# Optimization experiments

Measured on AMD Instinct MI355X. Metric: run time of the kernel, lower is better.

The kernel has to match this reference:

```python
import jax, jax.numpy as jnp
import numpy as np

# BitLinear (BitNet-style) constants, reconstructed from missing helpers:
#   get_qb_range(b) -> (-2^(b-1), 2^(b-1));  Qb = 2^(b-1) = 128 for bit_range=8
#   get_beta(W)  = mean(|W|)   (||W||_1 / (n*m))
#   get_gamma(W) = max(|W|)
QB = 128.0
EP = 0.01        # ep init arg: clip margin
LN_EPS = 1e-5    # nn.LayerNorm default eps
N_IN = 4096
N_OUT = 4096


def setup_inputs() -> dict:
    key = jax.random.key(0)
    kx, kw = jax.random.split(key, 2)
    x = jax.random.normal(kx, (4, 2048, N_IN), dtype=jnp.float32)
    # weight_init(): w0 ~ N(0,1); alpha = mean(w0); binarize sign(w0 - alpha)
    w0 = jax.random.normal(kw, (N_IN, N_OUT), dtype=jnp.float32)
    alpha = jnp.mean(w0)
    beta = jnp.mean(jnp.abs(w0))          # get_beta
    gamma = jnp.max(jnp.abs(w0))          # get_gamma
    w = jnp.where(w0 - alpha > 0, 1.0, -1.0).astype(jnp.float32)
    ln_gamma = jnp.ones((N_IN,), dtype=jnp.float32)   # LayerNorm weight
    ln_beta = jnp.zeros((N_IN,), dtype=jnp.float32)   # LayerNorm bias
    return {"x": x, "w": w, "ln_gamma": ln_gamma, "ln_beta": ln_beta,
            "beta": beta, "gamma": gamma}


def reference(x, w, ln_gamma, ln_beta, beta, gamma):
    # LayerNorm over last dim
    mu = jnp.mean(x, axis=-1, keepdims=True)
    var = jnp.mean(jnp.square(x - mu), axis=-1, keepdims=True)
    xn = (x - mu) * jax.lax.rsqrt(var + LN_EPS) * ln_gamma + ln_beta
    # ABSMax quantize: scale by Qb/gamma, clip to [-Qb+ep, Qb-ep] (no int cast)
    xq = jnp.clip(xn * (QB / gamma), -QB + EP, QB - EP)
    # binary-weight matmul + dequant scale beta*gamma/Qb
    y = jnp.einsum("bsi,io->bso", xq, w) * (beta * gamma / QB)
    return y
```

## Files before the change

### kernel.cpp

```cpp
#include <hip/hip_runtime.h>

using i32x4  = __attribute__((ext_vector_type(4))) int;
using i32x16 = __attribute__((ext_vector_type(16))) int;

constexpr int K_DIM = 4096;
constexpr int N_DIM = 4096;
constexpr float QBf = 128.0f;
constexpr float EPf = 0.01f;
constexpr float LN_EPSf = 1e-5f;

#define GLOAD_LDS16(gp, lp)                                                  \
    __builtin_amdgcn_global_load_lds(                                        \
        (const __attribute__((address_space(1))) void*)(gp),                 \
        (__attribute__((address_space(3))) void*)(lp), 16, 0, 0)

#define BARRIER()                                                            \
    do { asm volatile("" ::: "memory");                                      \
         __builtin_amdgcn_s_barrier();                                       \
         asm volatile("" ::: "memory"); } while (0)

#define WAIT_LGKM(N)                                                         \
    do { asm volatile("s_waitcnt lgkmcnt(" #N ")" ::: "memory");             \
         __builtin_amdgcn_sched_barrier(0); } while (0)

__global__ __launch_bounds__(256) void ln_quant_kernel(
    const float* __restrict__ x,
    const float* __restrict__ ln_g,
    const float* __restrict__ ln_b,
    const float* __restrict__ gamma_p,
    char* __restrict__ xq)
{
    const int row = blockIdx.x;
    const int t = threadIdx.x;
    const float4* xr4 = reinterpret_cast<const float4*>(x + (size_t)row * K_DIM);

    float4 v[4];
    float sum = 0.f, sumsq = 0.f;
#pragma unroll
    for (int i = 0; i < 4; ++i) {
        v[i] = xr4[t * 4 + i];
        sum += v[i].x + v[i].y + v[i].z + v[i].w;
        sumsq += v[i].x * v[i].x + v[i].y * v[i].y + v[i].z * v[i].z + v[i].w * v[i].w;
    }
#pragma unroll
    for (int off = 32; off > 0; off >>= 1) {
        sum += __shfl_down(sum, off);
        sumsq += __shfl_down(sumsq, off);
    }
    __shared__ float s_sum[4], s_sq[4];
    const int lane = t & 63, w = t >> 6;
    if (lane == 0) { s_sum[w] = sum; s_sq[w] = sumsq; }
    __syncthreads();
    sum = s_sum[0] + s_sum[1] + s_sum[2] + s_sum[3];
    sumsq = s_sq[0] + s_sq[1] + s_sq[2] + s_sq[3];

    const float mu = sum * (1.0f / K_DIM);
    const float var = sumsq * (1.0f / K_DIM) - mu * mu;
    const float rstd = rsqrtf(var + LN_EPSf);
    const float qs = QBf / gamma_p[0];
    const float lo = -QBf + EPf, hi = QBf - EPf;

    alignas(16) char ob[16];
#pragma unroll
    for (int i = 0; i < 4; ++i) {
        const float4 g = reinterpret_cast<const float4*>(ln_g)[t * 4 + i];
        const float4 b = reinterpret_cast<const float4*>(ln_b)[t * 4 + i];
        const float f0 = fminf(fmaxf(((v[i].x - mu) * rstd * g.x + b.x) * qs, lo), hi);
        const float f1 = fminf(fmaxf(((v[i].y - mu) * rstd * g.y + b.y) * qs, lo), hi);
        const float f2 = fminf(fmaxf(((v[i].z - mu) * rstd * g.z + b.z) * qs, lo), hi);
        const float f3 = fminf(fmaxf(((v[i].w - mu) * rstd * g.w + b.w) * qs, lo), hi);
        int x0 = (int)rintf(f0), x1 = (int)rintf(f1);
        int x2 = (int)rintf(f2), x3 = (int)rintf(f3);
        ob[i * 4 + 0] = (char)(x0 > 127 ? 127 : x0);
        ob[i * 4 + 1] = (char)(x1 > 127 ? 127 : x1);
        ob[i * 4 + 2] = (char)(x2 > 127 ? 127 : x2);
        ob[i * 4 + 3] = (char)(x3 > 127 ? 127 : x3);
    }
    *reinterpret_cast<uint4*>(xq + (size_t)row * K_DIM + t * 16) =
        *reinterpret_cast<const uint4*>(ob);
}

__global__ __launch_bounds__(256) void wtrans_kernel(
    const float* __restrict__ w, char* __restrict__ wq)
{
    __shared__ char tile[64][68];
    const int t = threadIdx.x;
    const int bk = blockIdx.y * 64;
    const int bn = blockIdx.x * 64;
#pragma unroll
    for (int i = 0; i < 4; ++i) {
        const int li = i * 1024 + t * 4;
        const int r = li >> 6, c = li & 63;
        const float4 vv = *reinterpret_cast<const float4*>(
            w + (size_t)(bk + r) * N_DIM + bn + c);
        tile[r][c]     = (char)vv.x;
        tile[r][c + 1] = (char)vv.y;
        tile[r][c + 2] = (char)vv.z;
        tile[r][c + 3] = (char)vv.w;
    }
    __syncthreads();
    const int n = t >> 2, kc = t & 3;
    alignas(16) char h16[16];
#pragma unroll
    for (int j = 0; j < 16; ++j) h16[j] = tile[kc * 16 + j][n];
    *reinterpret_cast<uint4*>(wq + (size_t)(bn + n) * K_DIM + bk + kc * 16) =
        *reinterpret_cast<const uint4*>(h16);
}

__global__ __launch_bounds__(512, 2) void gemm_kernel(
    const char* __restrict__ A,
    const char* __restrict__ Bt,
    float* __restrict__ C,
    const float* __restrict__ beta_p,
    const float* __restrict__ gamma_p)
{
    constexpr int NT = K_DIM / 64;
    __shared__ __align__(16) char lds[98304];

    const int t = threadIdx.x;
    const int flat = blockIdx.y * gridDim.x + blockIdx.x;
    const int xcd = flat & 7;
    const int r8 = flat >> 3;
    const int by = ((xcd >> 1) << 3) + (r8 >> 3);
    const int bx = ((xcd & 1) << 3) + (r8 & 7);
    const int bm = by * 256;
    const int bn = bx * 256;

    const int lane = t & 63;
    const int w = t >> 6;
    const int wm = w >> 2;
    const int wn = w & 3;
    const int ln31 = lane & 31;
    const int lg2 = lane >> 5;

    const char* gA = A + (size_t)bm * K_DIM;
    const char* gB = Bt + (size_t)bn * K_DIM;
    const int voff = (t & 255) * K_DIM + ((t >> 8) << 4);

    const int aoff = lg2 * 4096 + ((wm * 128 + ln31) << 4);
    const int boff = lg2 * 4096 + ((wn * 64 + ln31) << 4);

#define STAGE(B, kt)                                                          \
    do {                                                                      \
        GLOAD_LDS16(gA + (size_t)(kt) * 64 + voff,                            \
                    lds + (B) * 32768 + t * 16);                              \
        GLOAD_LDS16(gA + (size_t)(kt) * 64 + voff + 32,                       \
                    lds + (B) * 32768 + 8192 + t * 16);                       \
        GLOAD_LDS16(gB + (size_t)(kt) * 64 + voff,                            \
                    lds + (B) * 32768 + 16384 + t * 16);                      \
        GLOAD_LDS16(gB + (size_t)(kt) * 64 + voff + 32,                       \
                    lds + (B) * 32768 + 16384 + 8192 + t * 16);               \
    } while (0)

#define LD(p) (*reinterpret_cast<const i32x4*>(p))

#define READ_B(BUFI)                                                          \
    do {                                                                      \
        const char* bb_ = lds + (BUFI) * 32768 + 16384;                       \
        _Pragma("unroll")                                                     \
        for (int ks = 0; ks < 2; ++ks)                                        \
            _Pragma("unroll")                                                 \
            for (int nf = 0; nf < 2; ++nf)                                    \
                bfr[ks * 2 + nf] = LD(bb_ + ks * 8192 + nf * 512 + boff);     \
    } while (0)

#define READ_AH(PN, BUFI)                                                     \
    do {                                                                      \
        const char* an_ = lds + (BUFI) * 32768;                               \
        _Pragma("unroll")                                                     \
        for (int ks = 0; ks < 2; ++ks)                                        \
            _Pragma("unroll")                                                 \
            for (int mf = 0; mf < 4; ++mf)                                    \
                afr[PN][ks * 4 + mf] = LD(an_ + ks * 8192 + mf * 512 + aoff); \
    } while (0)

#define MFMA16(P)                                                             \
    do {                                                                      \
        __builtin_amdgcn_s_setprio(1);                                        \
        _Pragma("unroll")                                                     \
        for (int ks = 0; ks < 2; ++ks)                                        \
            _Pragma("unroll")                                                 \
            for (int mf = 0; mf < 4; ++mf)                                    \
                _Pragma("unroll")                                             \
                for (int nf = 0; nf < 2; ++nf)                                \
                    acc[mf][nf] = __builtin_amdgcn_mfma_i32_32x32x32_i8(      \
                        afr[P][ks * 4 + mf], bfr[ks * 2 + nf],                \
                        acc[mf][nf], 0, 0, 0);                                \
        __builtin_amdgcn_s_setprio(0);                                        \
    } while (0)

#define TILE(BC, BN_, BS, P, PN, RD, ST, tt)                                  \
    do {                                                                      \
        READ_B(BC);                                                           \
        if (RD) READ_AH(PN, BN_);                                             \
        if (ST) STAGE(BS, (tt) + 2);                                          \
        if (RD) { WAIT_LGKM(8); } else { WAIT_LGKM(0); }                      \
        MFMA16(P);                                                            \
        asm volatile("s_waitcnt vmcnt(0)" ::: "memory");                      \
        BARRIER();                                                            \
    } while (0)

    i32x16 acc[4][2];
#pragma unroll
    for (int m = 0; m < 4; ++m)
#pragma unroll
        for (int n = 0; n < 2; ++n)
#pragma unroll
            for (int q = 0; q < 16; ++q)
                acc[m][n][q] = 0;

    i32x4 afr[2][8];
    i32x4 bfr[4];

    STAGE(0, 0); STAGE(1, 1);
    asm volatile("s_waitcnt vmcnt(0)" ::: "memory");
    BARRIER();
    READ_AH(0, 0);

    for (int kt = 0; kt < NT - 4; kt += 6) {
        TILE(0, 1, 2, 0, 1, 1, 1, kt);
        TILE(1, 2, 0, 1, 0, 1, 1, kt + 1);
        TILE(2, 0, 1, 0, 1, 1, 1, kt + 2);
        TILE(0, 1, 2, 1, 0, 1, 1, kt + 3);
        TILE(1, 2, 0, 0, 1, 1, 1, kt + 4);
        TILE(2, 0, 1, 1, 0, 1, 1, kt + 5);
    }
    TILE(0, 1, 2, 0, 1, 1, 1, NT - 4);
    TILE(1, 2, 0, 1, 0, 1, 1, NT - 3);
    TILE(2, 0, 1, 0, 1, 1, 0, NT - 2);
    TILE(0, 1, 2, 1, 0, 0, 0, NT - 1);

    const float scale = beta_p[0] * gamma_p[0] * (1.0f / QBf);
    const int orow0 = bm + wm * 128 + lg2 * 4;
    const int ocol0 = bn + wn * 64 + ln31;
#pragma unroll
    for (int mf = 0; mf < 4; ++mf) {
#pragma unroll
        for (int nf = 0; nf < 2; ++nf) {
#pragma unroll
            for (int reg = 0; reg < 16; ++reg) {
                const int row = orow0 + mf * 32 + (reg & 3) + 8 * (reg >> 2);
                C[(size_t)row * N_DIM + ocol0 + nf * 32] =
                    (float)acc[mf][nf][reg] * scale;
            }
        }
    }
#undef STAGE
#undef LD
#undef READ_B
#undef READ_AH
#undef MFMA16
#undef TILE
}

extern "C" void kernel_launch(void* const* d_in, const int* in_sizes, int n_in,
                              void* d_out, int out_size, void* d_ws, size_t ws_size,
                              hipStream_t stream)
{
    const float* x       = (const float*)d_in[0];
    const float* w       = (const float*)d_in[1];
    const float* ln_g    = (const float*)d_in[2];
    const float* ln_b    = (const float*)d_in[3];
    const float* beta_p  = (const float*)d_in[4];
    const float* gamma_p = (const float*)d_in[5];
    float* out = (float*)d_out;

    const int M = in_sizes[0] / K_DIM;

    char* xq = (char*)d_ws;
    char* wq = (char*)d_ws + (size_t)M * K_DIM;

    ln_quant_kernel<<<M, 256, 0, stream>>>(x, ln_g, ln_b, gamma_p, xq);
    wtrans_kernel<<<dim3(N_DIM / 64, K_DIM / 64), 256, 0, stream>>>(w, wq);
    gemm_kernel<<<dim3(N_DIM / 256, M / 256), 512, 0, stream>>>(xq, wq, out, beta_p, gamma_p);
}
```

Measured before the change: 262.2 us.

## Split A/B LDS staging with deeper B prefetch and interleaved A-fragment reads

Restructures the int8 GEMM main loop so A and B tiles get separate LDS ring buffers. A is double-buffered, while B is quad-buffered and prefetched three tiles ahead. A fragments are now read in small chunks interleaved with groups of four MFMAs, and the next tile's B fragments are read ahead during the current tile. The waits on outstanding global loads are relaxed from vmcnt(0) to vmcnt(2). The aim is to cut register pressure from the large afr array and to hide LDS and global latency better, at the cost of more frequent lgkm waits and more complex buffer indexing.

```diff
diff --git a/kernel.cpp b/kernel.cpp
--- a/kernel.cpp
+++ b/kernel.cpp
@@ -140,63 +140,68 @@
     const int aoff = lg2 * 4096 + ((wm * 128 + ln31) << 4);
     const int boff = lg2 * 4096 + ((wn * 64 + ln31) << 4);
 
-#define STAGE(B, kt)                                                          \
+#define STAGE_A(abi, kt)                                                      \
     do {                                                                      \
         GLOAD_LDS16(gA + (size_t)(kt) * 64 + voff,                            \
-                    lds + (B) * 32768 + t * 16);                              \
+                    lds + (abi) * 16384 + t * 16);                            \
         GLOAD_LDS16(gA + (size_t)(kt) * 64 + voff + 32,                       \
-                    lds + (B) * 32768 + 8192 + t * 16);                       \
+                    lds + (abi) * 16384 + 8192 + t * 16);                     \
+    } while (0)
+
+#define STAGE_B(bbi, kt)                                                      \
+    do {                                                                      \
         GLOAD_LDS16(gB + (size_t)(kt) * 64 + voff,                            \
-                    lds + (B) * 32768 + 16384 + t * 16);                      \
+                    lds + 32768 + (bbi) * 16384 + t * 16);                    \
         GLOAD_LDS16(gB + (size_t)(kt) * 64 + voff + 32,                       \
-                    lds + (B) * 32768 + 16384 + 8192 + t * 16);               \
+                    lds + 32768 + (bbi) * 16384 + 8192 + t * 16);             \
     } while (0)
 
 #define LD(p) (*reinterpret_cast<const i32x4*>(p))
 
-#define READ_B(BUFI)                                                          \
-    do {                                                                      \
-        const char* bb_ = lds + (BUFI) * 32768 + 16384;                       \
+#define READ_A(par, ks, mfp)                                                  \
+    do {                                                                      \
+        afr[par][0] = LD(ab + (ks) * 8192 + ((mfp) * 2) * 512 + aoff);        \
+        afr[par][1] = LD(ab + (ks) * 8192 + ((mfp) * 2 + 1) * 512 + aoff);    \
+    } while (0)
+
+#define READ_BAHEAD(BNXT, bnbi)                                               \
+    do {                                                                      \
+        const char* bn_ = lds + 32768 + (bnbi) * 16384;                       \
         _Pragma("unroll")                                                     \
         for (int ks = 0; ks < 2; ++ks)                                        \
             _Pragma("unroll")                                                 \
             for (int nf = 0; nf < 2; ++nf)                                    \
-                bfr[ks * 2 + nf] = LD(bb_ + ks * 8192 + nf * 512 + boff);     \
-    } while (0)
-
-#define READ_AH(PN, BUFI)                                                     \
-    do {                                                                      \
-        const char* an_ = lds + (BUFI) * 32768;                               \
-        _Pragma("unroll")                                                     \
-        for (int ks = 0; ks < 2; ++ks)                                        \
-            _Pragma("unroll")                                                 \
-            for (int mf = 0; mf < 4; ++mf)                                    \
-                afr[PN][ks * 4 + mf] = LD(an_ + ks * 8192 + mf * 512 + aoff); \
-    } while (0)
-
-#define MFMA16(P)                                                             \
+                BNXT[ks * 2 + nf] = LD(bn_ + ks * 8192 + nf * 512 + boff);    \
+    } while (0)
+
+#define MFMA4(par, ks, mfp, BCUR)                                             \
     do {                                                                      \
         __builtin_amdgcn_s_setprio(1);                                        \
         _Pragma("unroll")                                                     \
-        for (int ks = 0; ks < 2; ++ks)                                        \
+        for (int m2 = 0; m2 < 2; ++m2)                                        \
             _Pragma("unroll")                                                 \
-            for (int mf = 0; mf < 4; ++mf)                                    \
-                _Pragma("unroll")                                             \
-                for (int nf = 0; nf < 2; ++nf)                                \
-                    acc[mf][nf] = __builtin_amdgcn_mfma_i32_32x32x32_i8(      \
-                        afr[P][ks * 4 + mf], bfr[ks * 2 + nf],                \
-                        acc[mf][nf], 0, 0, 0);                                \
+            for (int nf = 0; nf < 2; ++nf)                                    \
+                acc[(mfp) * 2 + m2][nf] =                                     \
+                    __builtin_amdgcn_mfma_i32_32x32x32_i8(                    \
+                        afr[par][m2], BCUR[(ks) * 2 + nf],                    \
+                        acc[(mfp) * 2 + m2][nf], 0, 0, 0);                    \
         __builtin_amdgcn_s_setprio(0);                                        \
     } while (0)
 
-#define TILE(BC, BN_, BS, P, PN, RD, ST, tt)                                  \
-    do {                                                                      \
-        READ_B(BC);                                                           \
-        if (RD) READ_AH(PN, BN_);                                             \
-        if (ST) STAGE(BS, (tt) + 2);                                          \
-        if (RD) { WAIT_LGKM(8); } else { WAIT_LGKM(0); }                      \
-        MFMA16(P);                                                            \
-        asm volatile("s_waitcnt vmcnt(0)" ::: "memory");                      \
+#define TILE(AB, SBB, BNB, BCUR, BNXT, STA, STB, RDB, VM, tt)                 \
+    do {                                                                      \
+        const char* ab = lds + (AB) * 16384;                                  \
+        READ_A(0, 0, 0);                                                      \
+         READ_A(1, 0, 1);                                             \
+        if (STA) STAGE_A((AB) ^ 1, (tt) + 1);                                 \
+        if (STB) STAGE_B(SBB, (tt) + 3);                                      \
+        WAIT_LGKM(2); MFMA4(0, 0, 0, BCUR);                                   \
+         READ_A(0, 1, 0); WAIT_LGKM(2); MFMA4(1, 0, 1, BCUR);         \
+         READ_A(1, 1, 1); WAIT_LGKM(2); MFMA4(0, 1, 0, BCUR);         \
+         if (RDB) { READ_BAHEAD(BNXT, BNB); WAIT_LGKM(4); }           \
+                 else     { WAIT_LGKM(0); }                                   \
+        MFMA4(1, 1, 1, BCUR);                                                 \
+        asm volatile("s_waitcnt vmcnt(" #VM ")" ::: "memory");                \
         BARRIER();                                                            \
     } while (0)
 
@@ -209,26 +214,24 @@
             for (int q = 0; q < 16; ++q)
                 acc[m][n][q] = 0;
 
-    i32x4 afr[2][8];
-    i32x4 bfr[4];
-
-    STAGE(0, 0); STAGE(1, 1);
-    asm volatile("s_waitcnt vmcnt(0)" ::: "memory");
+    i32x4 afr[2][2];
+    i32x4 bfrA[4], bfrB[4];
+
+    STAGE_A(0, 0); STAGE_B(0, 0); STAGE_B(1, 1); STAGE_B(2, 2);
+    asm volatile("s_waitcnt vmcnt(2)" ::: "memory");
     BARRIER();
-    READ_AH(0, 0);
-
-    for (int kt = 0; kt < NT - 4; kt += 6) {
-        TILE(0, 1, 2, 0, 1, 1, 1, kt);
-        TILE(1, 2, 0, 1, 0, 1, 1, kt + 1);
-        TILE(2, 0, 1, 0, 1, 1, 1, kt + 2);
-        TILE(0, 1, 2, 1, 0, 1, 1, kt + 3);
-        TILE(1, 2, 0, 0, 1, 1, 1, kt + 4);
-        TILE(2, 0, 1, 1, 0, 1, 1, kt + 5);
-    }
-    TILE(0, 1, 2, 0, 1, 1, 1, NT - 4);
-    TILE(1, 2, 0, 1, 0, 1, 1, NT - 3);
-    TILE(2, 0, 1, 0, 1, 1, 0, NT - 2);
-    TILE(0, 1, 2, 1, 0, 0, 0, NT - 1);
+    READ_BAHEAD(bfrA, 0);
+
+    for (int kt = 0; kt < NT - 4; kt += 4) {
+        TILE(0, 3, 1, bfrA, bfrB, 1, 1, 1, 2, kt);
+        TILE(1, 0, 2, bfrB, bfrA, 1, 1, 1, 2, kt + 1);
+        TILE(0, 1, 3, bfrA, bfrB, 1, 1, 1, 2, kt + 2);
+        TILE(1, 2, 0, bfrB, bfrA, 1, 1, 1, 2, kt + 3);
+    }
+    TILE(0, 3, 1, bfrA, bfrB, 1, 1, 1, 2, NT - 4);
+    TILE(1, 0, 2, bfrB, bfrA, 1, 0, 1, 0, NT - 3);
+    TILE(0, 1, 3, bfrA, bfrB, 1, 0, 1, 0, NT - 2);
+    TILE(1, 2, 0, bfrB, bfrA, 0, 0, 0, 0, NT - 1);
 
     const float scale = beta_p[0] * gamma_p[0] * (1.0f / QBf);
     const int orow0 = bm + wm * 128 + lg2 * 4;
@@ -245,11 +248,12 @@
             }
         }
     }
-#undef STAGE
+#undef STAGE_A
+#undef STAGE_B
 #undef LD
-#undef READ_B
-#undef READ_AH
-#undef MFMA16
+#undef READ_A
+#undef READ_BAHEAD
+#undef MFMA4
 #undef TILE
 }
 
```

Result: faster. 255.4 us (-2.6%).

## Switch int8 GEMM to double-buffered 128-wide K tiles with split A/B staging

Applied to the files above, without the earlier changes.

Replaces the triple-buffered 64-wide K pipeline with a double-buffered scheme using 128-wide K tiles and 128KB of LDS. Each tile runs two phases; the A half of the next tile is staged during the first and the B half during the second. This halves the number of outer iterations and tile barriers. The cost is that A fragments are no longer prefetched into registers across tiles. Each phase now waits for all LDS reads before its MFMAs, so LDS latency may be exposed.

```diff
diff --git a/kernel.cpp b/kernel.cpp
--- a/kernel.cpp
+++ b/kernel.cpp
@@ -19,8 +19,8 @@
          __builtin_amdgcn_s_barrier();                                       \
          asm volatile("" ::: "memory"); } while (0)
 
-#define WAIT_LGKM(N)                                                         \
-    do { asm volatile("s_waitcnt lgkmcnt(" #N ")" ::: "memory");             \
+#define WAIT_LGKM0()                                                         \
+    do { asm volatile("s_waitcnt lgkmcnt(0)" ::: "memory");                  \
          __builtin_amdgcn_sched_barrier(0); } while (0)
 
 __global__ __launch_bounds__(256) void ln_quant_kernel(
@@ -114,8 +114,8 @@
     const float* __restrict__ beta_p,
     const float* __restrict__ gamma_p)
 {
-    constexpr int NT = K_DIM / 64;
-    __shared__ __align__(16) char lds[98304];
+    constexpr int NT = K_DIM / 128;
+    __shared__ __align__(16) char lds[131072];
 
     const int t = threadIdx.x;
     const int flat = blockIdx.y * gridDim.x + blockIdx.x;
@@ -140,63 +140,69 @@
     const int aoff = lg2 * 4096 + ((wm * 128 + ln31) << 4);
     const int boff = lg2 * 4096 + ((wn * 64 + ln31) << 4);
 
-#define STAGE(B, kt)                                                          \
-    do {                                                                      \
-        GLOAD_LDS16(gA + (size_t)(kt) * 64 + voff,                            \
-                    lds + (B) * 32768 + t * 16);                              \
-        GLOAD_LDS16(gA + (size_t)(kt) * 64 + voff + 32,                       \
-                    lds + (B) * 32768 + 8192 + t * 16);                       \
-        GLOAD_LDS16(gB + (size_t)(kt) * 64 + voff,                            \
-                    lds + (B) * 32768 + 16384 + t * 16);                      \
-        GLOAD_LDS16(gB + (size_t)(kt) * 64 + voff + 32,                       \
-                    lds + (B) * 32768 + 16384 + 8192 + t * 16);               \
+#define STAGE_A(b, kt)                                                        \
+    do {                                                                      \
+        _Pragma("unroll")                                                     \
+        for (int r = 0; r < 4; ++r)                                           \
+            GLOAD_LDS16(gA + (size_t)(kt) * 128 + voff + r * 32,              \
+                        lds + (b) * 65536 + r * 8192 + t * 16);               \
+    } while (0)
+
+#define STAGE_B(b, kt)                                                        \
+    do {                                                                      \
+        _Pragma("unroll")                                                     \
+        for (int r = 0; r < 4; ++r)                                           \
+            GLOAD_LDS16(gB + (size_t)(kt) * 128 + voff + r * 32,              \
+                        lds + (b) * 65536 + 32768 + r * 8192 + t * 16);       \
     } while (0)
 
 #define LD(p) (*reinterpret_cast<const i32x4*>(p))
 
-#define READ_B(BUFI)                                                          \
-    do {                                                                      \
-        const char* bb_ = lds + (BUFI) * 32768 + 16384;                       \
-        _Pragma("unroll")                                                     \
-        for (int ks = 0; ks < 2; ++ks)                                        \
+#define READ_PH(ph)                                                           \
+    do {                                                                      \
+        _Pragma("unroll")                                                     \
+        for (int k2 = 0; k2 < 2; ++k2) {                                      \
+            _Pragma("unroll")                                                 \
+            for (int mf = 0; mf < 4; ++mf)                                    \
+                afr[k2][mf] = LD(ab + ((ph) * 2 + k2) * 8192 + mf * 512 + aoff); \
             _Pragma("unroll")                                                 \
             for (int nf = 0; nf < 2; ++nf)                                    \
-                bfr[ks * 2 + nf] = LD(bb_ + ks * 8192 + nf * 512 + boff);     \
-    } while (0)
-
-#define READ_AH(PN, BUFI)                                                     \
-    do {                                                                      \
-        const char* an_ = lds + (BUFI) * 32768;                               \
-        _Pragma("unroll")                                                     \
-        for (int ks = 0; ks < 2; ++ks)                                        \
-            _Pragma("unroll")                                                 \
-            for (int mf = 0; mf < 4; ++mf)                                    \
-                afr[PN][ks * 4 + mf] = LD(an_ + ks * 8192 + mf * 512 + aoff); \
-    } while (0)
-
-#define MFMA16(P)                                                             \
+                bfr[k2][nf] = LD(bb + ((ph) * 2 + k2) * 8192 + nf * 512 + boff); \
+        }                                                                     \
+    } while (0)
+
+#define MFMA_PH()                                                             \
     do {                                                                      \
         __builtin_amdgcn_s_setprio(1);                                        \
         _Pragma("unroll")                                                     \
-        for (int ks = 0; ks < 2; ++ks)                                        \
+        for (int k2 = 0; k2 < 2; ++k2)                                        \
             _Pragma("unroll")                                                 \
             for (int mf = 0; mf < 4; ++mf)                                    \
                 _Pragma("unroll")                                             \
                 for (int nf = 0; nf < 2; ++nf)                                \
                     acc[mf][nf] = __builtin_amdgcn_mfma_i32_32x32x32_i8(      \
-                        afr[P][ks * 4 + mf], bfr[ks * 2 + nf],                \
-                        acc[mf][nf], 0, 0, 0);                                \
+                        afr[k2][mf], bfr[k2][nf], acc[mf][nf], 0, 0, 0);      \
         __builtin_amdgcn_s_setprio(0);                                        \
     } while (0)
 
-#define TILE(BC, BN_, BS, P, PN, RD, ST, tt)                                  \
-    do {                                                                      \
-        READ_B(BC);                                                           \
-        if (RD) READ_AH(PN, BN_);                                             \
-        if (ST) STAGE(BS, (tt) + 2);                                          \
-        if (RD) { WAIT_LGKM(8); } else { WAIT_LGKM(0); }                      \
-        MFMA16(P);                                                            \
-        asm volatile("s_waitcnt vmcnt(0)" ::: "memory");                      \
+#define TILE(b, tt)                                                           \
+    do {                                                                      \
+        const char* ab = lds + (b) * 65536;                                   \
+        const char* bb = ab + 32768;                                          \
+        i32x4 afr[2][4], bfr[2][2];                                           \
+                                                         \
+        READ_PH(0);                                                           \
+        if ((tt) + 1 < NT) STAGE_A((b) ^ 1, (tt) + 1);                        \
+        BARRIER();                                                            \
+        WAIT_LGKM0();                                                         \
+        MFMA_PH();                                                            \
+                                                         \
+        READ_PH(1);                                                           \
+        if ((tt) + 1 < NT) STAGE_B((b) ^ 1, (tt) + 1);                        \
+        BARRIER();                                                            \
+        WAIT_LGKM0();                                                         \
+        MFMA_PH();                                                            \
+        if ((tt) + 1 < NT) asm volatile("s_waitcnt vmcnt(0)" ::: "memory");   \
         BARRIER();                                                            \
     } while (0)
 
@@ -209,26 +215,14 @@
             for (int q = 0; q < 16; ++q)
                 acc[m][n][q] = 0;
 
-    i32x4 afr[2][8];
-    i32x4 bfr[4];
-
-    STAGE(0, 0); STAGE(1, 1);
+    STAGE_A(0, 0); STAGE_B(0, 0);
     asm volatile("s_waitcnt vmcnt(0)" ::: "memory");
     BARRIER();
-    READ_AH(0, 0);
-
-    for (int kt = 0; kt < NT - 4; kt += 6) {
-        TILE(0, 1, 2, 0, 1, 1, 1, kt);
-        TILE(1, 2, 0, 1, 0, 1, 1, kt + 1);
-        TILE(2, 0, 1, 0, 1, 1, 1, kt + 2);
-        TILE(0, 1, 2, 1, 0, 1, 1, kt + 3);
-        TILE(1, 2, 0, 0, 1, 1, 1, kt + 4);
-        TILE(2, 0, 1, 1, 0, 1, 1, kt + 5);
-    }
-    TILE(0, 1, 2, 0, 1, 1, 1, NT - 4);
-    TILE(1, 2, 0, 1, 0, 1, 1, NT - 3);
-    TILE(2, 0, 1, 0, 1, 1, 0, NT - 2);
-    TILE(0, 1, 2, 1, 0, 0, 0, NT - 1);
+
+    for (int kt = 0; kt < NT; kt += 2) {
+        TILE(0, kt);
+        TILE(1, kt + 1);
+    }
 
     const float scale = beta_p[0] * gamma_p[0] * (1.0f / QBf);
     const int orow0 = bm + wm * 128 + lg2 * 4;
@@ -245,11 +239,11 @@
             }
         }
     }
-#undef STAGE
+#undef STAGE_A
+#undef STAGE_B
 #undef LD
-#undef READ_B
-#undef READ_AH
-#undef MFMA16
+#undef READ_PH
+#undef MFMA_PH
 #undef TILE
 }
 
```

Result: faster. 249.4 us (-4.9%).
